# Performance work log

Measured on AMD Instinct MI355X. Metric: run time of the kernel, lower is better.

## Reference

```python
import jax, jax.numpy as jnp
import numpy as np


def setup_inputs() -> dict:
    key = jax.random.key(0)
    k1, k2 = jax.random.split(key)
    B, N = 4096, 2048
    mid = jax.random.normal(k1, (B, N), dtype=jnp.float32)
    half = jax.random.uniform(k2, (B, N), dtype=jnp.float32) * 0.5
    l = mid - half  # lower bound
    u = mid + half  # upper bound (l <= u elementwise)
    return {"l": l, "u": u}


def reference(l, u):
    # Original torch code builds (B, n, n) tensors: for the lower bound, row i is
    # u[b, :] with entry i replaced by l[b, i]; it softmaxes each row and extracts
    # the diagonal. Diagonal of that softmax equals:
    #   lower[b, i] = exp(l[b,i]) / (exp(l[b,i]) + sum_{j != i} exp(u[b,j]))
    # and symmetrically for the upper bound. Softmax is shift-invariant, so we
    # stabilize with a per-row global max M and use the sum-exclude-one trick,
    # computing the exact same math in O(B*n) instead of O(B*n^2).
    M = jnp.maximum(jnp.max(l, axis=-1, keepdims=True),
                    jnp.max(u, axis=-1, keepdims=True))  # (B, 1)
    e_l = jnp.exp(l - M)  # (B, n)
    e_u = jnp.exp(u - M)  # (B, n)
    S_l = jnp.sum(e_l, axis=-1, keepdims=True)  # (B, 1)
    S_u = jnp.sum(e_u, axis=-1, keepdims=True)  # (B, 1)
    lower_result = e_l / (e_l + (S_u - e_u))  # diag of softmax(lower rows)
    upper_result = e_u / (e_u + (S_l - e_l))  # diag of softmax(upper rows)
    return lower_result, upper_result
```

## Files before the change

### kernel.cpp

```cpp
#include <hip/hip_runtime.h>

#define BLOCK 256
#define NCOL 2048

typedef float f32x4 __attribute__((ext_vector_type(4)));

__device__ __forceinline__ float waveReduceMax(float v) {
#pragma unroll
    for (int o = 32; o > 0; o >>= 1) v = fmaxf(v, __shfl_xor(v, o, 64));
    return v;
}
__device__ __forceinline__ float waveReduceSum(float v) {
#pragma unroll
    for (int o = 32; o > 0; o >>= 1) v += __shfl_xor(v, o, 64);
    return v;
}

__global__ __launch_bounds__(BLOCK) void interval_softmax_kernel(
    const float* __restrict__ L, const float* __restrict__ U,
    float* __restrict__ lo, float* __restrict__ up)
{
    const int row  = blockIdx.x;
    const int tid  = threadIdx.x;
    const int wave = tid >> 6;
    const int lane = tid & 63;

    const f32x4* L4 = reinterpret_cast<const f32x4*>(L) + (size_t)row * (NCOL / 4);
    const f32x4* U4 = reinterpret_cast<const f32x4*>(U) + (size_t)row * (NCOL / 4);

    f32x4 a0 = L4[tid];
    f32x4 a1 = L4[tid + BLOCK];
    f32x4 b0 = U4[tid];
    f32x4 b1 = U4[tid + BLOCK];

    float m = fmaxf(fmaxf(fmaxf(a0.x, a0.y), fmaxf(a0.z, a0.w)),
                    fmaxf(fmaxf(a1.x, a1.y), fmaxf(a1.z, a1.w)));
    m = fmaxf(m, fmaxf(fmaxf(fmaxf(b0.x, b0.y), fmaxf(b0.z, b0.w)),
                       fmaxf(fmaxf(b1.x, b1.y), fmaxf(b1.z, b1.w))));
    m = waveReduceMax(m);

    __shared__ float smax[4];
    __shared__ float ssl[4];
    __shared__ float ssu[4];
    if (lane == 0) smax[wave] = m;
    __syncthreads();
    m = fmaxf(fmaxf(smax[0], smax[1]), fmaxf(smax[2], smax[3]));

    f32x4 el0, el1, eu0, eu1;
    el0.x = __expf(a0.x - m); el0.y = __expf(a0.y - m);
    el0.z = __expf(a0.z - m); el0.w = __expf(a0.w - m);
    el1.x = __expf(a1.x - m); el1.y = __expf(a1.y - m);
    el1.z = __expf(a1.z - m); el1.w = __expf(a1.w - m);
    eu0.x = __expf(b0.x - m); eu0.y = __expf(b0.y - m);
    eu0.z = __expf(b0.z - m); eu0.w = __expf(b0.w - m);
    eu1.x = __expf(b1.x - m); eu1.y = __expf(b1.y - m);
    eu1.z = __expf(b1.z - m); eu1.w = __expf(b1.w - m);

    float sl = (el0.x + el0.y) + (el0.z + el0.w) + (el1.x + el1.y) + (el1.z + el1.w);
    float su = (eu0.x + eu0.y) + (eu0.z + eu0.w) + (eu1.x + eu1.y) + (eu1.z + eu1.w);
    sl = waveReduceSum(sl);
    su = waveReduceSum(su);
    if (lane == 0) { ssl[wave] = sl; ssu[wave] = su; }
    __syncthreads();
    sl = (ssl[0] + ssl[1]) + (ssl[2] + ssl[3]);
    su = (ssu[0] + ssu[1]) + (ssu[2] + ssu[3]);

    f32x4 o0, o1;
    o0.x = __fdividef(el0.x, el0.x + (su - eu0.x));
    o0.y = __fdividef(el0.y, el0.y + (su - eu0.y));
    o0.z = __fdividef(el0.z, el0.z + (su - eu0.z));
    o0.w = __fdividef(el0.w, el0.w + (su - eu0.w));
    o1.x = __fdividef(el1.x, el1.x + (su - eu1.x));
    o1.y = __fdividef(el1.y, el1.y + (su - eu1.y));
    o1.z = __fdividef(el1.z, el1.z + (su - eu1.z));
    o1.w = __fdividef(el1.w, el1.w + (su - eu1.w));

    f32x4* lo4 = reinterpret_cast<f32x4*>(lo) + (size_t)row * (NCOL / 4);
    __builtin_nontemporal_store(o0, &lo4[tid]);
    __builtin_nontemporal_store(o1, &lo4[tid + BLOCK]);

    f32x4 p0, p1;
    p0.x = __fdividef(eu0.x, eu0.x + (sl - el0.x));
    p0.y = __fdividef(eu0.y, eu0.y + (sl - el0.y));
    p0.z = __fdividef(eu0.z, eu0.z + (sl - el0.z));
    p0.w = __fdividef(eu0.w, eu0.w + (sl - el0.w));
    p1.x = __fdividef(eu1.x, eu1.x + (sl - el1.x));
    p1.y = __fdividef(eu1.y, eu1.y + (sl - el1.y));
    p1.z = __fdividef(eu1.z, eu1.z + (sl - el1.z));
    p1.w = __fdividef(eu1.w, eu1.w + (sl - el1.w));

    f32x4* up4 = reinterpret_cast<f32x4*>(up) + (size_t)row * (NCOL / 4);
    __builtin_nontemporal_store(p0, &up4[tid]);
    __builtin_nontemporal_store(p1, &up4[tid + BLOCK]);
}

extern "C" void kernel_launch(void* const* d_in, const int* in_sizes, int n_in,
                              void* d_out, int out_size, void* d_ws, size_t ws_size,
                              hipStream_t stream) {
    const float* L = (const float*)d_in[0];
    const float* U = (const float*)d_in[1];
    const int rows = in_sizes[0] / NCOL;
    float* lo = (float*)d_out;
    float* up = lo + (size_t)rows * NCOL;
    interval_softmax_kernel<<<rows, BLOCK, 0, stream>>>(L, U, lo, up);
}
```

Measured before the change: 25.25 us.

## Assign one row per wavefront to drop block-level shared-memory reductions

Each 64-lane wavefront now handles a whole row, keeping 8 float4 chunks of L and U per lane in registers, so the max and the sums are computed with wave shuffles only. This removes the two __syncthreads barriers and the LDS traffic of the block-wide reductions, and the grid shrinks by a factor of four. In exchange each lane holds more live registers (64 floats of input), which may reduce occupancy, and the launch assumes the row count is a multiple of four.

```diff
diff --git a/kernel.cpp b/kernel.cpp
--- a/kernel.cpp
+++ b/kernel.cpp
@@ -1,7 +1,9 @@
 #include <hip/hip_runtime.h>
 
+#define NCOL 2048
+#define VEC_PER_ROW (NCOL / 4)
+#define PER_LANE 8
 #define BLOCK 256
-#define NCOL 2048
 
 typedef float f32x4 __attribute__((ext_vector_type(4)));
 
@@ -20,78 +22,56 @@
     const float* __restrict__ L, const float* __restrict__ U,
     float* __restrict__ lo, float* __restrict__ up)
 {
-    const int row  = blockIdx.x;
-    const int tid  = threadIdx.x;
-    const int wave = tid >> 6;
-    const int lane = tid & 63;
+    const int wave = threadIdx.x >> 6;
+    const int lane = threadIdx.x & 63;
+    const int row  = blockIdx.x * (BLOCK / 64) + wave;
 
-    const f32x4* L4 = reinterpret_cast<const f32x4*>(L) + (size_t)row * (NCOL / 4);
-    const f32x4* U4 = reinterpret_cast<const f32x4*>(U) + (size_t)row * (NCOL / 4);
+    const f32x4* L4 = reinterpret_cast<const f32x4*>(L) + (size_t)row * VEC_PER_ROW;
+    const f32x4* U4 = reinterpret_cast<const f32x4*>(U) + (size_t)row * VEC_PER_ROW;
 
-    f32x4 a0 = L4[tid];
-    f32x4 a1 = L4[tid + BLOCK];
-    f32x4 b0 = U4[tid];
-    f32x4 b1 = U4[tid + BLOCK];
+    f32x4 a[PER_LANE], b[PER_LANE];
+#pragma unroll
+    for (int k = 0; k < PER_LANE; ++k) a[k] = L4[lane + 64 * k];
+#pragma unroll
+    for (int k = 0; k < PER_LANE; ++k) b[k] = U4[lane + 64 * k];
 
-    float m = fmaxf(fmaxf(fmaxf(a0.x, a0.y), fmaxf(a0.z, a0.w)),
-                    fmaxf(fmaxf(a1.x, a1.y), fmaxf(a1.z, a1.w)));
-    m = fmaxf(m, fmaxf(fmaxf(fmaxf(b0.x, b0.y), fmaxf(b0.z, b0.w)),
-                       fmaxf(fmaxf(b1.x, b1.y), fmaxf(b1.z, b1.w))));
+    float m = -3.402823466e38f;
+#pragma unroll
+    for (int k = 0; k < PER_LANE; ++k) {
+        m = fmaxf(m, fmaxf(fmaxf(a[k].x, a[k].y), fmaxf(a[k].z, a[k].w)));
+        m = fmaxf(m, fmaxf(fmaxf(b[k].x, b[k].y), fmaxf(b[k].z, b[k].w)));
+    }
     m = waveReduceMax(m);
 
-    __shared__ float smax[4];
-    __shared__ float ssl[4];
-    __shared__ float ssu[4];
-    if (lane == 0) smax[wave] = m;
-    __syncthreads();
-    m = fmaxf(fmaxf(smax[0], smax[1]), fmaxf(smax[2], smax[3]));
-
-    f32x4 el0, el1, eu0, eu1;
-    el0.x = __expf(a0.x - m); el0.y = __expf(a0.y - m);
-    el0.z = __expf(a0.z - m); el0.w = __expf(a0.w - m);
-    el1.x = __expf(a1.x - m); el1.y = __expf(a1.y - m);
-    el1.z = __expf(a1.z - m); el1.w = __expf(a1.w - m);
-    eu0.x = __expf(b0.x - m); eu0.y = __expf(b0.y - m);
-    eu0.z = __expf(b0.z - m); eu0.w = __expf(b0.w - m);
-    eu1.x = __expf(b1.x - m); eu1.y = __expf(b1.y - m);
-    eu1.z = __expf(b1.z - m); eu1.w = __expf(b1.w - m);
-
-    float sl = (el0.x + el0.y) + (el0.z + el0.w) + (el1.x + el1.y) + (el1.z + el1.w);
-    float su = (eu0.x + eu0.y) + (eu0.z + eu0.w) + (eu1.x + eu1.y) + (eu1.z + eu1.w);
+    float sl = 0.f, su = 0.f;
+#pragma unroll
+    for (int k = 0; k < PER_LANE; ++k) {
+        a[k].x = __expf(a[k].x - m); a[k].y = __expf(a[k].y - m);
+        a[k].z = __expf(a[k].z - m); a[k].w = __expf(a[k].w - m);
+        b[k].x = __expf(b[k].x - m); b[k].y = __expf(b[k].y - m);
+        b[k].z = __expf(b[k].z - m); b[k].w = __expf(b[k].w - m);
+        sl += (a[k].x + a[k].y) + (a[k].z + a[k].w);
+        su += (b[k].x + b[k].y) + (b[k].z + b[k].w);
+    }
     sl = waveReduceSum(sl);
     su = waveReduceSum(su);
-    if (lane == 0) { ssl[wave] = sl; ssu[wave] = su; }
-    __syncthreads();
-    sl = (ssl[0] + ssl[1]) + (ssl[2] + ssl[3]);
-    su = (ssu[0] + ssu[1]) + (ssu[2] + ssu[3]);
 
-    f32x4 o0, o1;
-    o0.x = __fdividef(el0.x, el0.x + (su - eu0.x));
-    o0.y = __fdividef(el0.y, el0.y + (su - eu0.y));
-    o0.z = __fdividef(el0.z, el0.z + (su - eu0.z));
-    o0.w = __fdividef(el0.w, el0.w + (su - eu0.w));
-    o1.x = __fdividef(el1.x, el1.x + (su - eu1.x));
-    o1.y = __fdividef(el1.y, el1.y + (su - eu1.y));
-    o1.z = __fdividef(el1.z, el1.z + (su - eu1.z));
-    o1.w = __fdividef(el1.w, el1.w + (su - eu1.w));
-
-    f32x4* lo4 = reinterpret_cast<f32x4*>(lo) + (size_t)row * (NCOL / 4);
-    __builtin_nontemporal_store(o0, &lo4[tid]);
-    __builtin_nontemporal_store(o1, &lo4[tid + BLOCK]);
-
-    f32x4 p0, p1;
-    p0.x = __fdividef(eu0.x, eu0.x + (sl - el0.x));
-    p0.y = __fdividef(eu0.y, eu0.y + (sl - el0.y));
-    p0.z = __fdividef(eu0.z, eu0.z + (sl - el0.z));
-    p0.w = __fdividef(eu0.w, eu0.w + (sl - el0.w));
-    p1.x = __fdividef(eu1.x, eu1.x + (sl - el1.x));
-    p1.y = __fdividef(eu1.y, eu1.y + (sl - el1.y));
-    p1.z = __fdividef(eu1.z, eu1.z + (sl - el1.z));
-    p1.w = __fdividef(eu1.w, eu1.w + (sl - el1.w));
-
-    f32x4* up4 = reinterpret_cast<f32x4*>(up) + (size_t)row * (NCOL / 4);
-    __builtin_nontemporal_store(p0, &up4[tid]);
-    __builtin_nontemporal_store(p1, &up4[tid + BLOCK]);
+    f32x4* lo4 = reinterpret_cast<f32x4*>(lo) + (size_t)row * VEC_PER_ROW;
+    f32x4* up4 = reinterpret_cast<f32x4*>(up) + (size_t)row * VEC_PER_ROW;
+#pragma unroll
+    for (int k = 0; k < PER_LANE; ++k) {
+        f32x4 o, p;
+        o.x = __fdividef(a[k].x, a[k].x + (su - b[k].x));
+        o.y = __fdividef(a[k].y, a[k].y + (su - b[k].y));
+        o.z = __fdividef(a[k].z, a[k].z + (su - b[k].z));
+        o.w = __fdividef(a[k].w, a[k].w + (su - b[k].w));
+        p.x = __fdividef(b[k].x, b[k].x + (sl - a[k].x));
+        p.y = __fdividef(b[k].y, b[k].y + (sl - a[k].y));
+        p.z = __fdividef(b[k].z, b[k].z + (sl - a[k].z));
+        p.w = __fdividef(b[k].w, b[k].w + (sl - a[k].w));
+        __builtin_nontemporal_store(o, &lo4[lane + 64 * k]);
+        __builtin_nontemporal_store(p, &up4[lane + 64 * k]);
+    }
 }
 
 extern "C" void kernel_launch(void* const* d_in, const int* in_sizes, int n_in,
@@ -102,5 +82,6 @@
     const int rows = in_sizes[0] / NCOL;
     float* lo = (float*)d_out;
     float* up = lo + (size_t)rows * NCOL;
-    interval_softmax_kernel<<<rows, BLOCK, 0, stream>>>(L, U, lo, up);
+    const int rows_per_block = BLOCK / 64;
+    interval_softmax_kernel<<<rows / rows_per_block, BLOCK, 0, stream>>>(L, U, lo, up);
 }
```

Result: no change. 25.65 us (+1.6%).
